# Kernel tuning notes

Hardware: AMD Instinct MI355X
Metric: run time of the kernel (lower is better)

Reference implementation:

```python
import jax, jax.numpy as jnp
import numpy as np

MAX_REL = 14
HEADS = 12
HEAD_DIM = 64
SCALE = HEAD_DIM ** -0.5


def _rel_indices(length):
    # Replicates ElasticRelativePosition2D index construction (static, numpy).
    L = length - 1
    s = int(L ** 0.5)
    r = np.arange(L)
    dv = r[None, :] // s - r[:, None] // s
    dh = r[None, :] % s - r[:, None] % s
    iv = np.clip(dv, -MAX_REL, MAX_REL) + MAX_REL + 1
    ih = np.clip(dh, -MAX_REL, MAX_REL) + MAX_REL + 1
    # pad top row and left col with index 0 (the CLS slot)
    iv = np.pad(iv, ((1, 0), (1, 0)), constant_values=0)
    ih = np.pad(ih, ((1, 0), (1, 0)), constant_values=0)
    return jnp.asarray(iv, dtype=jnp.int32), jnp.asarray(ih, dtype=jnp.int32)


def _rel_emb(table_v, table_h, length):
    iv, ih = _rel_indices(length)
    return table_v[iv] + table_h[ih]  # [length, length, 64]


def setup_inputs() -> dict:
    key = jax.random.key(0)
    ks = jax.random.split(key, 16)
    B, L, D = 32, 577, 768
    T = 2 * MAX_REL + 2  # 30
    std = 0.02
    inp = {
        "q": jax.random.normal(ks[0], (B, L, D), jnp.float32),
        "k": jax.random.normal(ks[1], (B, L, D), jnp.float32),
        "v": jax.random.normal(ks[2], (B, L, D), jnp.float32),
        "Wq": jax.random.normal(ks[3], (D, HEADS * HEAD_DIM), jnp.float32) * std,
        "bq": jnp.zeros((HEADS * HEAD_DIM,), jnp.float32),
        "Wk": jax.random.normal(ks[4], (D, HEADS * HEAD_DIM), jnp.float32) * std,
        "bk": jnp.zeros((HEADS * HEAD_DIM,), jnp.float32),
        "Wv": jax.random.normal(ks[5], (D, HEADS * HEAD_DIM), jnp.float32) * std,
        "bv": jnp.zeros((HEADS * HEAD_DIM,), jnp.float32),
        "Wp": jax.random.normal(ks[6], (HEADS * HEAD_DIM, D), jnp.float32) * std,
        "bp": jnp.zeros((D,), jnp.float32),
        "tab_vk": jax.random.normal(ks[7], (T, HEAD_DIM), jnp.float32) * std,
        "tab_hk": jax.random.normal(ks[8], (T, HEAD_DIM), jnp.float32) * std,
        "tab_vv": jax.random.normal(ks[9], (T, HEAD_DIM), jnp.float32) * std,
        "tab_hv": jax.random.normal(ks[10], (T, HEAD_DIM), jnp.float32) * std,
    }
    return inp


def reference(q, k, v, Wq, bq, Wk, bk, Wv, bv, Wp, bp, tab_vk, tab_hk, tab_vv, tab_hv):
    B, L, D = q.shape
    residual = q
    qh = (q @ Wq + bq).reshape(B, L, HEADS, HEAD_DIM).transpose(0, 2, 1, 3)  # [B,H,L,d]
    kh = (k @ Wk + bk).reshape(B, L, HEADS, HEAD_DIM).transpose(0, 2, 1, 3)
    vh = (v @ Wv + bv).reshape(B, L, HEADS, HEAD_DIM).transpose(0, 2, 1, 3)

    attn = jnp.einsum("bhid,bhjd->bhij", qh, kh) * SCALE
    r_p_k = _rel_emb(tab_vk, tab_hk, L)  # [L,L,d]
    attn = attn + jnp.einsum("bhid,ijd->bhij", qh, r_p_k)  # bias NOT scaled (as in source)
    attn = jax.nn.softmax(attn, axis=-1)

    out = jnp.einsum("bhij,bhjd->bhid", attn, vh)
    r_p_v = _rel_emb(tab_vv, tab_hv, L)
    out = out + jnp.einsum("bhij,ijd->bhid", attn, r_p_v)
    out = out.transpose(0, 2, 1, 3).reshape(B, L, HEADS * HEAD_DIM)

    out = out @ Wp + bp
    return out + residual
```

## Files before the change

kernel.cpp:

```cpp
#include <hip/hip_runtime.h>
#include <cstdint>


typedef unsigned short u16;
typedef unsigned int   u32;
typedef __attribute__((ext_vector_type(8))) __bf16 bf16x8;
typedef __attribute__((ext_vector_type(4))) float  f32x4;

#define B_   32
#define L_   577
#define D_   768
#define H_   12
#define HD_  64
#define LP_  640
#define M_   (B_*L_)
#define SCALE_ 0.125f

__device__ __forceinline__ float b2f(u16 u){ u32 x = ((u32)u) << 16; float f; __builtin_memcpy(&f,&x,4); return f; }
__device__ __forceinline__ u16 f2b(float f){ u32 x; __builtin_memcpy(&x,&f,4); u32 r = (x + 0x7FFFu + ((x>>16)&1u)) >> 16; return (u16)r; }

__device__ __forceinline__ f32x4 mfma_bf16(bf16x8 a, bf16x8 b, f32x4 c){
  return __builtin_amdgcn_mfma_f32_16x16x32_bf16(a, b, c, 0, 0, 0);
}

__device__ __forceinline__ void async16(const void* g, void* l){
  __builtin_amdgcn_global_load_lds(
    (const __attribute__((address_space(1))) void*)g,
    (__attribute__((address_space(3))) void*)l,
    16, 0, 0);
}

__device__ __forceinline__ void lds_fence(){
  asm volatile("s_waitcnt lgkmcnt(0)" ::: "memory");
}

__global__ __launch_bounds__(256) void ind_setup(u16* __restrict__ ind)
{
  int jt = blockIdx.x;
  int t  = threadIdx.x;
  int nt = t >> 6, lane = t & 63;
  int qq = lane >> 4, cc = lane & 15;
  int n = nt*16 + cc;
  u16 vals[8];
  #pragma unroll
  for (int idx = 0; idx < 8; ++idx){
    int j = jt*32 + qq*8 + idx;
    int bv, bhh;
    if (j == 0){ bv = 24; bhh = 24; }
    else { int jj = j-1; bv = jj/24; if (bv > 23) bv = 23; bhh = jj - (jj/24)*24; }
    bool one = (n < 25) ? (bv == n) : ((n < 50) ? (bhh == n-25) : false);
    vals[idx] = one ? (u16)0x3F80 : (u16)0;
  }
  *(uint4*)&ind[(size_t)((jt*4 + nt)*64 + lane)*8] = *(uint4*)vals;
}

__global__ __launch_bounds__(256) void tab_setup(
    const float* __restrict__ tvk, const float* __restrict__ thk,
    const float* __restrict__ tvv, const float* __restrict__ thv,
    u16* __restrict__ tabK, u16* __restrict__ tabVT)
{
  int i = blockIdx.x*256 + threadIdx.x;
  if (i >= 64*64) return;
  int r = i >> 6, col = i & 63;
  float kv = 0.f;
  if (r < 30)      kv = tvk[r*HD_ + col];
  else if (r < 60) kv = thk[(r-30)*HD_ + col];
  tabK[i] = f2b(kv);
  float vv = 0.f;
  if (col < 30)      vv = tvv[col*HD_ + r];
  else if (col < 60) vv = thv[(col-30)*HD_ + r];
  tabVT[i] = f2b(vv);
}

__global__ __launch_bounds__(256) void cvt3_bf16(
    const float* __restrict__ q, const float* __restrict__ k, const float* __restrict__ v,
    u16* __restrict__ dq, u16* __restrict__ dk, u16* __restrict__ dv)
{
  int z = blockIdx.y;
  const float* s = (z==0)?q:(z==1)?k:v;
  u16*         d = (z==0)?dq:(z==1)?dk:dv;
  int i = blockIdx.x*256 + threadIdx.x;
  if (i >= (M_*D_)/8) return;
  const float4* s4 = (const float4*)s;
  float4 a = s4[2*i], b = s4[2*i+1];
  uint4 o;
  o.x = (u32)f2b(a.x) | ((u32)f2b(a.y)<<16);
  o.y = (u32)f2b(a.z) | ((u32)f2b(a.w)<<16);
  o.z = (u32)f2b(b.x) | ((u32)f2b(b.y)<<16);
  o.w = (u32)f2b(b.z) | ((u32)f2b(b.w)<<16);
  ((uint4*)d)[i] = o;
}

__global__ __launch_bounds__(256) void transpose768(
    const float* __restrict__ W0, const float* __restrict__ W1,
    const float* __restrict__ W2, const float* __restrict__ W3,
    u16* __restrict__ T0, u16* __restrict__ T1, u16* __restrict__ T2, u16* __restrict__ T3)
{
  __shared__ float t[32][33];
  int z = blockIdx.z;
  const float* W = (z==0)?W0:(z==1)?W1:(z==2)?W2:W3;
  u16*         T = (z==0)?T0:(z==1)?T1:(z==2)?T2:T3;
  int kb = blockIdx.x*32, nb = blockIdx.y*32;
  int tx = threadIdx.x & 31, ty = threadIdx.x >> 5;
  #pragma unroll
  for (int r=0;r<32;r+=8) t[ty+r][tx] = W[(size_t)(kb+ty+r)*768 + nb+tx];
  __syncthreads();
  #pragma unroll
  for (int r=0;r<32;r+=8) T[(size_t)(nb+ty+r)*768 + kb+tx] = f2b(t[tx][ty+r]);
}

__global__ __launch_bounds__(256) void vtr_kernel(
    const u16* __restrict__ vh, u16* __restrict__ vhT)
{
  __shared__ __align__(16) u16 t[64][72];
  int ll0 = blockIdx.x * 64;
  size_t bhs = (size_t)(blockIdx.z*H_ + blockIdx.y) * LP_ * HD_;
  const u16* src = vh + bhs;
  u16* dst = vhT + bhs;
  int tid = threadIdx.x;
  #pragma unroll
  for (int it=0; it<2; ++it){
    int idx = it*256 + tid;
    int row = idx >> 3, ch = (idx & 7)*8;
    uint4 d4; d4.x=0u; d4.y=0u; d4.z=0u; d4.w=0u;
    if (ll0 + row < L_) d4 = *(const uint4*)(src + (size_t)(ll0+row)*HD_ + ch);
    *(uint4*)&t[row][ch] = d4;
  }
  __syncthreads();
  #pragma unroll
  for (int it=0; it<2; ++it){
    int idx = it*256 + tid;
    int dd = idx >> 3, l8 = (idx & 7)*8;
    u16 vals[8];
    #pragma unroll
    for (int e=0;e<8;++e) vals[e] = t[l8+e][dd];
    *(uint4*)(dst + (size_t)dd*LP_ + ll0 + l8) = *(uint4*)vals;
  }
}

__global__ __launch_bounds__(256) void gemm_kernel(
    const u16* __restrict__ A, const u16* __restrict__ BT,
    const float* __restrict__ bias, const float* __restrict__ resid,
    void* __restrict__ Dstv, int mode)
{
  __shared__ __align__(16) u16 AsL[128*32];
  __shared__ __align__(16) u16 BsL[128*32];
  const int blk = blockIdx.x;
  const int x = blk & 7, g = blk >> 3;
  const int n0 = (g % 6) * 128;
  const int m_idx = (g / 6) * 8 + x;
  if (m_idx >= 145) return;
  const int m0 = m_idx * 128;

  const int tid = threadIdx.x;
  const int w = tid>>6, lane = tid&63, q = lane>>4, c = lane&15;
  const int wr = w>>1, wc = w&1;

  f32x4 acc[4][4];
  #pragma unroll
  for (int ai=0;ai<4;++ai)
    #pragma unroll
    for (int bi=0;bi<4;++bi){ f32x4 z = {0.f,0.f,0.f,0.f}; acc[ai][bi] = z; }

  for (int k0 = 0; k0 < 768; k0 += 32){
    __syncthreads();
    #pragma unroll
    for (int t2 = 0; t2 < 2; ++t2){
      int idx = t2*256 + tid;
      int row = idx >> 2, ch = idx & 3;
      int mrow = m0 + row; if (mrow > M_-1) mrow = M_-1;
      const u16* srcA;
      if (mode < 3) srcA = A + (size_t)mrow*768 + k0 + ch*8;
      else {
        int bb = mrow / L_, ll = mrow - bb*L_;
        int hh = k0 >> 6, dd = (k0 & 63) + ch*8;
        srcA = A + (((size_t)(bb*H_ + hh)*LP_ + ll) << 6) + dd;
      }
      async16(srcA, (char*)AsL + (size_t)(t2*256 + w*64)*16);
      async16(BT + (size_t)(n0 + row)*768 + k0 + ch*8, (char*)BsL + (size_t)(t2*256 + w*64)*16);
    }
    __syncthreads();

    bf16x8 af[4], bf2[4];
    #pragma unroll
    for (int ai=0;ai<4;++ai) af[ai]  = *(const bf16x8*)&AsL[(wr*64 + ai*16 + c)*32 + q*8];
    #pragma unroll
    for (int bi=0;bi<4;++bi) bf2[bi] = *(const bf16x8*)&BsL[(wc*64 + bi*16 + c)*32 + q*8];
    #pragma unroll
    for (int ai=0;ai<4;++ai)
      #pragma unroll
      for (int bi=0;bi<4;++bi)
        acc[ai][bi] = mfma_bf16(af[ai], bf2[bi], acc[ai][bi]);
  }

  #pragma unroll
  for (int ai=0;ai<4;++ai){
    #pragma unroll
    for (int r2=0;r2<4;++r2){
      int mrow = m0 + wr*64 + ai*16 + q*4 + r2;
      if (mrow >= M_) continue;
      int bb = mrow / L_;
      int ll = mrow - bb*L_;
      #pragma unroll
      for (int bi=0;bi<4;++bi){
        int col = n0 + wc*64 + bi*16 + c;
        float vv = acc[ai][bi][r2] + bias[col];
        if (mode < 3){
          int hh = col >> 6, dd = col & 63;
          ((u16*)Dstv)[(((size_t)(bb*H_ + hh)*LP_ + ll) << 6) + dd] = f2b(vv);
        } else {
          size_t o2 = (size_t)mrow*768 + col;
          ((float*)Dstv)[o2] = vv + resid[o2];
        }
      }
    }
  }
}

__global__ __launch_bounds__(256) void attn_kernel(
    const u16* __restrict__ qh, const u16* __restrict__ kh, const u16* __restrict__ vhT,
    const u16* __restrict__ tabK, const u16* __restrict__ tabVT,
    const u16* __restrict__ ind,
    u16* __restrict__ oh)
{
  __shared__ __align__(16) char sb[4*6720];
  const int tid = threadIdx.x;
  const int w = tid>>6, lane = tid&63, q = lane>>4, c = lane&15;
  char* wb = sb + w*6720;
  float* gvh  = (float*)wb;
  u16*   Ps_w = (u16*)(wb + 3328);
  u16*   pvhb = (u16*)(wb + 4608);

  const int id = blockIdx.x;
  const int lin = (id & 7)*480 + (id >> 3);
  const int qt = lin % 10;
  const int hb = lin / 10;
  const int h = hb % 12, b = hb / 12;

  const int i0 = qt * 64;
  const size_t bh = (size_t)(b*H_ + h) * LP_ * HD_;
  const u16* qh_b = qh + bh;
  const u16* kh_b = kh + bh;
  const u16* vT_b = vhT + bh;

  bf16x8 aq0 = *(const bf16x8*)(qh_b + (size_t)(i0 + w*16 + c)*HD_ + q*8);
  bf16x8 aq1 = *(const bf16x8*)(qh_b + (size_t)(i0 + w*16 + c)*HD_ + 32 + q*8);

  #pragma unroll
  for (int nt=0; nt<4; ++nt){
    bf16x8 tb0 = *(const bf16x8*)(tabK + (size_t)(nt*16+c)*64 + q*8);
    bf16x8 tb1 = *(const bf16x8*)(tabK + (size_t)(nt*16+c)*64 + 32 + q*8);
    f32x4 s = {0.f,0.f,0.f,0.f};
    s = mfma_bf16(aq0, tb0, s);
    s = mfma_bf16(aq1, tb1, s);
    int bin = nt*16 + c;
    if (bin < 60){
      #pragma unroll
      for (int r=0;r<4;++r) pvhb[(q*4+r)*66 + bin] = f2b(s[r]);
    }
  }
  lds_fence();

  int rv_[4], cv_[4], ig_[4];
  #pragma unroll
  for (int r=0;r<4;++r){
    int ig = i0 + w*16 + q*4 + r;
    ig_[r] = ig;
    int ii = ig > 0 ? ig - 1 : 0;
    int dv24 = ii / 24;
    rv_[r] = dv24;
    cv_[r] = ii - dv24*24;
  }
  float pv0[4], ph0[4];
  #pragma unroll
  for (int r=0;r<4;++r){
    int lr = q*4 + r;
    pv0[r] = b2f(pvhb[lr*66 + 0]);
    ph0[r] = b2f(pvhb[lr*66 + 30]);
  }

  f32x4 o4[4], hist[4];
  #pragma unroll
  for (int nt=0;nt<4;++nt){ f32x4 z = {0.f,0.f,0.f,0.f}; o4[nt] = z; hist[nt] = z; }

  for (int jt = 0; jt < 19; ++jt){
    int j0 = jt * 32;
    uint4 bi_raw[4];
    #pragma unroll
    for (int nt=0;nt<4;++nt) bi_raw[nt] = ((const uint4*)ind)[(jt*4 + nt)*64 + lane];

    lds_fence();
    #pragma unroll
    for (int sub=0; sub<2; ++sub){
      const u16* kr = kh_b + (size_t)(j0 + sub*16 + c)*HD_;
      bf16x8 bk0 = *(const bf16x8*)(kr + q*8);
      bf16x8 bk1 = *(const bf16x8*)(kr + 32 + q*8);
      f32x4 s4 = {0.f,0.f,0.f,0.f};
      s4 = mfma_bf16(aq0, bk0, s4);
      s4 = mfma_bf16(aq1, bk1, s4);

      int jbase = j0 + sub*16;
      int j  = jbase + c;
      bool jv = (j < L_);
      int jj = j - 1;
      int gR  = (j==0) ? 24 : (jj/24);  if (gR > 23 && j != 0) gR = 23;
      int cbR = (j==0) ? 24 : (jj - (jj/24)*24);
      int sga = (jbase <= 1) ? 0 : ((jbase-1)/24); if (sga > 23) sga = 23;
      int sgb = (jbase + 14) / 24;                 if (sgb > 23) sgb = 23;

      #pragma unroll
      for (int r=0;r<4;++r){
        int lr = q*4 + r;
        int dvlo = sga - rv_[r]; dvlo = dvlo < -14 ? -14 : (dvlo > 14 ? 14 : dvlo);
        int dvhi = sgb - rv_[r]; dvhi = dvhi < -14 ? -14 : (dvhi > 14 ? 14 : dvhi);
        float bvlo = b2f(pvhb[lr*66 + dvlo + 15]);
        float bvhi = b2f(pvhb[lr*66 + dvhi + 15]);
        float bv = (gR == sgb) ? bvhi : bvlo;
        int dh = cbR - cv_[r]; dh = dh < -14 ? -14 : (dh > 14 ? 14 : dh);
        float bhh = b2f(pvhb[lr*66 + dh + 45]);
        bool cls = (j == 0) || (ig_[r] == 0);
        float bias = (cls ? pv0[r] : bv) + (cls ? ph0[r] : bhh);
        float s = s4[r]*SCALE_ + bias;
        s = fminf(fmaxf(s, -80.f), 30.f);
        float p = jv ? __expf(s) : 0.f;
        Ps_w[lr*40 + sub*16 + c] = f2b(p);
      }
    }
    lds_fence();
    bf16x8 ap = *(const bf16x8*)(Ps_w + c*40 + q*8);
    #pragma unroll
    for (int nt=0;nt<4;++nt){
      bf16x8 bv2 = *(const bf16x8*)(vT_b + (size_t)(nt*16+c)*LP_ + j0 + q*8);
      o4[nt] = mfma_bf16(ap, bv2, o4[nt]);
      bf16x8 bI = *(const bf16x8*)&bi_raw[nt];
      hist[nt] = mfma_bf16(ap, bI, hist[nt]);
    }
  }

  #pragma unroll
  for (int nt=0;nt<4;++nt){
    int bin = nt*16 + c;
    if (bin < 50){
      #pragma unroll
      for (int r=0;r<4;++r)
        gvh[(size_t)(q*4 + r)*52 + bin] = hist[nt][r];
    }
  }
  lds_fence();

  u16* Wm = (u16*)(wb + 3328);
  for (int o = lane; o < 16*72; o += 64) Wm[o] = 0;
  lds_fence();
  if (lane < 16){
    int ig = i0 + w*16 + lane;
    const float* gv = gvh + (size_t)lane*52;
    u16* wrp = Wm + lane*72;
    if (ig == 0){
      float sv=0.f, sh=0.f;
      for (int g2=0; g2<25; ++g2){ sv += gv[g2]; sh += gv[25+g2]; }
      wrp[0] = f2b(sv); wrp[30] = f2b(sh);
    } else {
      int rr = (ig-1)/24, cc2 = (ig-1) - ((ig-1)/24)*24;
      wrp[0]  = f2b(gv[24]);
      wrp[30] = f2b(gv[49]);
      for (int t=1; t<30; ++t){
        float sv = 0.f, sh = 0.f;
        if (t == 1){
          for (int g2=0; g2 <= rr-14  && g2 < 24; ++g2) sv += gv[g2];
          for (int c2=0; c2 <= cc2-14 && c2 < 24; ++c2) sh += gv[25+c2];
        } else if (t == 29){
          for (int g2 = (rr+14  < 0 ? 0 : rr+14 ); g2 < 24; ++g2) sv += gv[g2];
          for (int c2 = (cc2+14 < 0 ? 0 : cc2+14); c2 < 24; ++c2) sh += gv[25+c2];
        } else {
          int g2 = rr  + t - 15; if (g2 >= 0 && g2 < 24) sv = gv[g2];
          int c2 = cc2 + t - 15; if (c2 >= 0 && c2 < 24) sh = gv[25+c2];
        }
        wrp[t] = f2b(sv); wrp[30+t] = f2b(sh);
      }
    }
  }
  lds_fence();

  bf16x8 aw0 = *(const bf16x8*)(Wm + c*72 + q*8);
  bf16x8 aw1 = *(const bf16x8*)(Wm + c*72 + 32 + q*8);
  #pragma unroll
  for (int nt=0;nt<4;++nt){
    bf16x8 bt0 = *(const bf16x8*)(tabVT + (size_t)(nt*16+c)*64 + q*8);
    bf16x8 bt1 = *(const bf16x8*)(tabVT + (size_t)(nt*16+c)*64 + 32 + q*8);
    o4[nt] = mfma_bf16(aw0, bt0, o4[nt]);
    o4[nt] = mfma_bf16(aw1, bt1, o4[nt]);
  }

  u16* oh_b = oh + bh;
  #pragma unroll
  for (int r=0;r<4;++r){
    if (ig_[r] < L_){
      const float* gr = gvh + (size_t)(q*4 + r)*52;
      f32x4 a0 = *(const f32x4*)(gr);
      f32x4 a1 = *(const f32x4*)(gr+4);
      f32x4 a2 = *(const f32x4*)(gr+8);
      f32x4 a3 = *(const f32x4*)(gr+12);
      f32x4 a4 = *(const f32x4*)(gr+16);
      f32x4 a5 = *(const f32x4*)(gr+20);
      float lsum = (a0[0]+a0[1]+a0[2]+a0[3]) + (a1[0]+a1[1]+a1[2]+a1[3])
                 + (a2[0]+a2[1]+a2[2]+a2[3]) + (a3[0]+a3[1]+a3[2]+a3[3])
                 + (a4[0]+a4[1]+a4[2]+a4[3]) + (a5[0]+a5[1]+a5[2]+a5[3]) + gr[24];
      float inv = 1.f / lsum;
      #pragma unroll
      for (int nt=0;nt<4;++nt)
        oh_b[(size_t)ig_[r]*HD_ + nt*16 + c] = f2b(o4[nt][r] * inv);
    }
  }
}

extern "C" void kernel_launch(void* const* d_in, const int* in_sizes, int n_in,
                              void* d_out, int out_size, void* d_ws, size_t ws_size,
                              hipStream_t stream)
{
  (void)in_sizes; (void)n_in; (void)out_size; (void)ws_size;
  const float* q_   = (const float*)d_in[0];
  const float* k_   = (const float*)d_in[1];
  const float* v_   = (const float*)d_in[2];
  const float* Wq_  = (const float*)d_in[3];
  const float* bq_  = (const float*)d_in[4];
  const float* Wk_  = (const float*)d_in[5];
  const float* bk_  = (const float*)d_in[6];
  const float* Wv_  = (const float*)d_in[7];
  const float* bv_  = (const float*)d_in[8];
  const float* Wp_  = (const float*)d_in[9];
  const float* bp_  = (const float*)d_in[10];
  const float* tvk_ = (const float*)d_in[11];
  const float* thk_ = (const float*)d_in[12];
  const float* tvv_ = (const float*)d_in[13];
  const float* thv_ = (const float*)d_in[14];

  char* ws = (char*)d_ws;
  const size_t szHead = (size_t)B_*H_*LP_*HD_*2;
  const size_t szQKV  = (size_t)M_*D_*2;
  u16* qh   = (u16*)(ws);
  u16* kh   = (u16*)(ws + szHead);
  u16* vh   = (u16*)(ws + 2*szHead);
  u16* oh   = (u16*)(ws + 3*szHead);
  u16* q_bf = oh;
  u16* k_bf = (u16*)(ws + 4*szHead);
  u16* v_bf = (u16*)(ws + 4*szHead + szQKV);
  u16* vhT  = k_bf;
  u16* WqT  = (u16*)(ws + 4*szHead + 2*szQKV);
  u16* WkT  = WqT + 768*768;
  u16* WvT  = WkT + 768*768;
  u16* WpT  = WvT + 768*768;
  u16* ind  = WpT + 768*768;
  u16* tabK  = ind + 19*4*64*8;
  u16* tabVT = tabK + 64*64;

  ind_setup<<<19, 256, 0, stream>>>(ind);
  tab_setup<<<16, 256, 0, stream>>>(tvk_, thk_, tvv_, thv_, tabK, tabVT);
  transpose768<<<dim3(24,24,4), 256, 0, stream>>>(Wq_, Wk_, Wv_, Wp_, WqT, WkT, WvT, WpT);
  cvt3_bf16<<<dim3((M_*D_/8 + 255)/256, 3), 256, 0, stream>>>(q_, k_, v_, q_bf, k_bf, v_bf);
  gemm_kernel<<<912, 256, 0, stream>>>(q_bf, WqT, bq_, nullptr, qh, 0);
  gemm_kernel<<<912, 256, 0, stream>>>(k_bf, WkT, bk_, nullptr, kh, 1);
  gemm_kernel<<<912, 256, 0, stream>>>(v_bf, WvT, bv_, nullptr, vh, 2);
  vtr_kernel<<<dim3(10,12,32), 256, 0, stream>>>(vh, vhT);
  attn_kernel<<<3840, 256, 0, stream>>>(qh, kh, vhT, tabK, tabVT, ind, oh);
  gemm_kernel<<<912, 256, 0, stream>>>(oh, WpT, bp_, q_, d_out, 3);
}
```

Before: 870.6 us.

## Precompute per-row bias table in LDS and prefetch V tiles early

Before the key loop, each warp builds a per-query-row table of 50 bias values (24 vertical groups plus CLS, 24 horizontal columns plus CLS), so the inner loop needs only two LDS lookups per score instead of clamp and select logic. V tile loads are issued at the top of each iteration so their latency overlaps the QK MFMAs, and s_setprio is raised around the MFMA blocks. Per-warp LDS shrinks because the bias table reuses the histogram region, and the bf16 conversion now uses a native cast. The extra LDS fence and setup loop add a small fixed cost per block.

After: 868.5 us. No clear change (-0.2%).

```diff
diff --git a/kernel.cpp b/kernel.cpp
--- a/kernel.cpp
+++ b/kernel.cpp
@@ -223,13 +223,14 @@
     const u16* __restrict__ ind,
     u16* __restrict__ oh)
 {
-  __shared__ __align__(16) char sb[4*6720];
+  __shared__ __align__(16) char sb[4*6272];
   const int tid = threadIdx.x;
   const int w = tid>>6, lane = tid&63, q = lane>>4, c = lane&15;
-  char* wb = sb + w*6720;
-  float* gvh  = (float*)wb;
-  u16*   Ps_w = (u16*)(wb + 3328);
-  u16*   pvhb = (u16*)(wb + 4608);
+  char* wb = sb + w*6272;
+  float* gvh   = (float*)wb;
+  u16*   pvhb  = (u16*)wb;
+  u16*   Ps_w  = (u16*)(wb + 3328);
+  u16*   bias_t= (u16*)(wb + 4608);
 
   const int id = blockIdx.x;
   const int lin = (id & 7)*480 + (id >> 3);
@@ -261,81 +262,93 @@
   }
   lds_fence();
 
-  int rv_[4], cv_[4], ig_[4];
-  #pragma unroll
-  for (int r=0;r<4;++r){
-    int ig = i0 + w*16 + q*4 + r;
-    ig_[r] = ig;
-    int ii = ig > 0 ? ig - 1 : 0;
-    int dv24 = ii / 24;
-    rv_[r] = dv24;
-    cv_[r] = ii - dv24*24;
-  }
-  float pv0[4], ph0[4];
-  #pragma unroll
-  for (int r=0;r<4;++r){
-    int lr = q*4 + r;
-    pv0[r] = b2f(pvhb[lr*66 + 0]);
-    ph0[r] = b2f(pvhb[lr*66 + 30]);
-  }
+  for (int o = lane; o < 16*50; o += 64){
+    int row = o / 50, t = o - (o/50)*50;
+    int ig = i0 + w*16 + row;
+    const u16* src = pvhb + row*66;
+    u16 val;
+    if (ig == 0){
+      val = src[t < 25 ? 0 : 30];
+    } else {
+      int im1 = ig - 1;
+      int rr = im1 / 24, cc2 = im1 - (im1/24)*24;
+      if (t < 25){
+        if (t == 24) val = src[0];
+        else { int d = t - rr;  d = d < -14 ? -14 : (d > 14 ? 14 : d); val = src[15 + d]; }
+      } else {
+        int cb = t - 25;
+        if (cb == 24) val = src[30];
+        else { int d = cb - cc2; d = d < -14 ? -14 : (d > 14 ? 14 : d); val = src[45 + d]; }
+      }
+    }
+    bias_t[row*52 + t] = val;
+  }
+  lds_fence();
+
+  int ig_[4];
+  #pragma unroll
+  for (int r=0;r<4;++r) ig_[r] = i0 + w*16 + q*4 + r;
 
   f32x4 o4[4], hist[4];
   #pragma unroll
   for (int nt=0;nt<4;++nt){ f32x4 z = {0.f,0.f,0.f,0.f}; o4[nt] = z; hist[nt] = z; }
+
+  const u16* btr = bias_t + (q*4)*52;
 
   for (int jt = 0; jt < 19; ++jt){
     int j0 = jt * 32;
+    lds_fence();
+
+    bf16x8 bvf[4];
+    #pragma unroll
+    for (int nt=0;nt<4;++nt)
+      bvf[nt] = *(const bf16x8*)(vT_b + (size_t)(nt*16+c)*LP_ + j0 + q*8);
     uint4 bi_raw[4];
     #pragma unroll
     for (int nt=0;nt<4;++nt) bi_raw[nt] = ((const uint4*)ind)[(jt*4 + nt)*64 + lane];
 
-    lds_fence();
     #pragma unroll
     for (int sub=0; sub<2; ++sub){
       const u16* kr = kh_b + (size_t)(j0 + sub*16 + c)*HD_;
       bf16x8 bk0 = *(const bf16x8*)(kr + q*8);
       bf16x8 bk1 = *(const bf16x8*)(kr + 32 + q*8);
       f32x4 s4 = {0.f,0.f,0.f,0.f};
+      __builtin_amdgcn_s_setprio(1);
       s4 = mfma_bf16(aq0, bk0, s4);
       s4 = mfma_bf16(aq1, bk1, s4);
-
-      int jbase = j0 + sub*16;
-      int j  = jbase + c;
+      __builtin_amdgcn_s_setprio(0);
+
+      int j  = j0 + sub*16 + c;
       bool jv = (j < L_);
       int jj = j - 1;
-      int gR  = (j==0) ? 24 : (jj/24);  if (gR > 23 && j != 0) gR = 23;
-      int cbR = (j==0) ? 24 : (jj - (jj/24)*24);
-      int sga = (jbase <= 1) ? 0 : ((jbase-1)/24); if (sga > 23) sga = 23;
-      int sgb = (jbase + 14) / 24;                 if (sgb > 23) sgb = 23;
+      int q24 = jj / 24;
+      int gR  = (j==0) ? 24 : (q24 > 23 ? 23 : q24);
+      int cbR = (j==0) ? 24 : (jj - q24*24);
 
       #pragma unroll
       for (int r=0;r<4;++r){
-        int lr = q*4 + r;
-        int dvlo = sga - rv_[r]; dvlo = dvlo < -14 ? -14 : (dvlo > 14 ? 14 : dvlo);
-        int dvhi = sgb - rv_[r]; dvhi = dvhi < -14 ? -14 : (dvhi > 14 ? 14 : dvhi);
-        float bvlo = b2f(pvhb[lr*66 + dvlo + 15]);
-        float bvhi = b2f(pvhb[lr*66 + dvhi + 15]);
-        float bv = (gR == sgb) ? bvhi : bvlo;
-        int dh = cbR - cv_[r]; dh = dh < -14 ? -14 : (dh > 14 ? 14 : dh);
-        float bhh = b2f(pvhb[lr*66 + dh + 45]);
-        bool cls = (j == 0) || (ig_[r] == 0);
-        float bias = (cls ? pv0[r] : bv) + (cls ? ph0[r] : bhh);
-        float s = s4[r]*SCALE_ + bias;
+        float bias = b2f(btr[r*52 + gR]) + b2f(btr[r*52 + 25 + cbR]);
+        float s = fmaf(s4[r], SCALE_, bias);
         s = fminf(fmaxf(s, -80.f), 30.f);
         float p = jv ? __expf(s) : 0.f;
-        Ps_w[lr*40 + sub*16 + c] = f2b(p);
+        __bf16 pb = (__bf16)p;
+        u16 pu; __builtin_memcpy(&pu, &pb, 2);
+        Ps_w[(q*4+r)*40 + sub*16 + c] = pu;
       }
     }
     lds_fence();
     bf16x8 ap = *(const bf16x8*)(Ps_w + c*40 + q*8);
+    __builtin_amdgcn_s_setprio(1);
     #pragma unroll
     for (int nt=0;nt<4;++nt){
-      bf16x8 bv2 = *(const bf16x8*)(vT_b + (size_t)(nt*16+c)*LP_ + j0 + q*8);
-      o4[nt] = mfma_bf16(ap, bv2, o4[nt]);
+      o4[nt] = mfma_bf16(ap, bvf[nt], o4[nt]);
       bf16x8 bI = *(const bf16x8*)&bi_raw[nt];
       hist[nt] = mfma_bf16(ap, bI, hist[nt]);
     }
-  }
+    __builtin_amdgcn_s_setprio(0);
+  }
+
+  lds_fence();
 
   #pragma unroll
   for (int nt=0;nt<4;++nt){
@@ -383,6 +396,7 @@
 
   bf16x8 aw0 = *(const bf16x8*)(Wm + c*72 + q*8);
   bf16x8 aw1 = *(const bf16x8*)(Wm + c*72 + 32 + q*8);
+  __builtin_amdgcn_s_setprio(1);
   #pragma unroll
   for (int nt=0;nt<4;++nt){
     bf16x8 bt0 = *(const bf16x8*)(tabVT + (size_t)(nt*16+c)*64 + q*8);
@@ -390,6 +404,7 @@
     o4[nt] = mfma_bf16(aw0, bt0, o4[nt]);
     o4[nt] = mfma_bf16(aw1, bt1, o4[nt]);
   }
+  __builtin_amdgcn_s_setprio(0);
 
   u16* oh_b = oh + bh;
   #pragma unroll
```
